# Performance work log

Hardware: AMD Instinct MI355X
Metric: run time of the kernel (lower is better)

## Reference

```python
import jax, jax.numpy as jnp
import numpy as np

E = 1024   # embedding_size
H = 16     # num_heads
DH = E // H


def setup_inputs() -> dict:
    key = jax.random.key(0)
    ks = jax.random.split(key, 11)
    B, S = 2, 2048
    std = 0.02
    return {
        "query": jax.random.normal(ks[0], (B, S, E), jnp.float32),
        "key": jax.random.normal(ks[1], (B, S, E), jnp.float32),
        "value": jax.random.normal(ks[2], (B, S, E), jnp.float32),
        "Wq": jax.random.normal(ks[3], (E, E), jnp.float32) * std,
        "bq": jnp.zeros((E,), jnp.float32),
        "Wk": jax.random.normal(ks[4], (E, E), jnp.float32) * std,
        "bk": jnp.zeros((E,), jnp.float32),
        "Wv": jax.random.normal(ks[5], (E, E), jnp.float32) * std,
        "bv": jnp.zeros((E,), jnp.float32),
        "Wo": jax.random.normal(ks[6], (E, E), jnp.float32) * std,
        "bo": jnp.zeros((E,), jnp.float32),
    }


def _split_heads(x, B, S):
    # [B,S,E] -> [B,H,S,DH]
    return x.reshape(B, S, H, DH).transpose(0, 2, 1, 3)


def reference(query, key, value, Wq, bq, Wk, bk, Wv, bv, Wo, bo):
    B, S, _ = query.shape
    # torch Linear: y = x @ W.T + b
    q = _split_heads(query @ Wq.T + bq, B, S)
    k = _split_heads(key @ Wk.T + bk, B, key.shape[1])
    v = _split_heads(value @ Wv.T + bv, B, value.shape[1])
    # naive unscaled attention (original has no 1/sqrt(d) factor)
    scores = jnp.einsum("bhsd,bhtd->bhst", q, k)  # [B,H,S,T]
    attn = jax.nn.softmax(scores, axis=-1)
    out = jnp.einsum("bhst,bhtd->bhsd", attn, v)  # [B,H,S,DH]
    out = out.transpose(0, 2, 1, 3).reshape(B, S, E)
    return out @ Wo.T + bo
```

## Files before the change

### kernel.cpp

```cpp
#include <hip/hip_runtime.h>
#include <hip/hip_bf16.h>

constexpr int kB   = 2;
constexpr int kS   = 2048;
constexpr int kE   = 1024;
constexpr int kH   = 16;
constexpr int kDH  = 64;
constexpr int kTok = kB * kS;

constexpr float kLog2e = 1.4426950408889634f;

typedef short bf16x8 __attribute__((ext_vector_type(8)));
typedef float f32x4  __attribute__((ext_vector_type(4)));
typedef unsigned int uint2v __attribute__((ext_vector_type(2)));

__device__ __forceinline__ float bf2f(unsigned short s) {
  union { unsigned int u; float f; } c; c.u = ((unsigned int)s) << 16; return c.f;
}
__device__ __forceinline__ unsigned short f2bf(float f) {
  union { float f; unsigned int u; } c; c.f = f;
  unsigned int u = c.u;
  u += 0x7fffu + ((u >> 16) & 1u);
  return (unsigned short)(u >> 16);
}

__device__ __forceinline__ unsigned cvtpk(float lo, float hi) {
  unsigned r;
  asm("v_cvt_pk_bf16_f32 %0, %1, %2" : "=v"(r) : "v"(lo), "v"(hi));
  return r;
}

__device__ __forceinline__ float fexp2(float x) {
  float r;
  asm("v_exp_f32 %0, %1" : "=v"(r) : "v"(x));
  return r;
}

__device__ __forceinline__ void gl_lds16(const unsigned short* g, unsigned short* l) {
  __builtin_amdgcn_global_load_lds(
      (const __attribute__((address_space(1))) unsigned int*)g,
      (__attribute__((address_space(3))) unsigned int*)l, 16, 0, 0);
}

__global__ void detect_dtype(const unsigned short* __restrict__ q, int* flag) {
  __shared__ int cnt;
  if (threadIdx.x == 0) cnt = 0;
  __syncthreads();
  int bad = 0;
  for (int i = threadIdx.x; i < 4096; i += 256) {
    unsigned int e = (q[i] >> 7) & 0xFF;
    if (e >= 0xC0) bad++;
  }
  atomicAdd(&cnt, bad);
  __syncthreads();
  if (threadIdx.x == 0) *flag = (cnt > 8) ? 1 : 0;
}

struct Seg { const void* src; unsigned short* dst; unsigned int n; unsigned int blk0; };
struct ConvArgs { Seg s[11]; float scale[11]; };

__global__ __launch_bounds__(256) void conv_all(ConvArgs a, const int* __restrict__ flag) {
  const unsigned int bid = blockIdx.x;
  int si = 0;
  #pragma unroll
  for (int i = 1; i < 11; ++i)
    if (bid >= a.s[i].blk0) si = i;
  const Seg sg = a.s[si];
  const float sc = a.scale[si];
  const int i0 = ((int)(bid - sg.blk0) * 256 + threadIdx.x) * 8;
  if (i0 >= (int)sg.n) return;
  if (*flag) {
    const float* s = (const float*)sg.src + i0;
    f32x4 f0 = *(const f32x4*)(s);
    f32x4 f1 = *(const f32x4*)(s + 4);
    bf16x8 v;
    #pragma unroll
    for (int j = 0; j < 4; ++j) v[j]     = (short)f2bf(f0[j] * sc);
    #pragma unroll
    for (int j = 0; j < 4; ++j) v[j + 4] = (short)f2bf(f1[j] * sc);
    *(bf16x8*)&sg.dst[i0] = v;
  } else {
    bf16x8 v = *(const bf16x8*)((const unsigned short*)sg.src + i0);
    if (sc != 1.0f) {
      #pragma unroll
      for (int j = 0; j < 8; ++j)
        v[j] = (short)f2bf(bf2f((unsigned short)v[j]) * sc);
    }
    *(bf16x8*)&sg.dst[i0] = v;
  }
}

__device__ __forceinline__ void gemm_core(
    const unsigned short* __restrict__ A,
    const unsigned short* __restrict__ W,
    int Kdim, int bM, int bN,
    unsigned short* As, unsigned short* Ws,
    f32x4 acc[4][4])
{
  const int tid  = threadIdx.x;
  const int lane = tid & 63;
  const int wv   = tid >> 6;
  const int wm   = (wv >> 1) * 64;
  const int wn   = (wv & 1) * 64;
  const int lr   = lane & 15;
  const int kq   = (lane >> 4) * 8;

  const int r0 = tid >> 2;
  const int c0 = (tid & 3) * 8;

  const unsigned short* Ag = A + (size_t)(bM + r0) * Kdim + c0;
  const unsigned short* Wg = W + (size_t)(bN + r0) * Kdim + c0;
  unsigned short* lA = &As[tid * 8];
  unsigned short* lW = &Ws[tid * 8];

  gl_lds16(Ag,                      lA);
  gl_lds16(Ag + (size_t)64 * Kdim,  lA + 2048);
  gl_lds16(Wg,                      lW);
  gl_lds16(Wg + (size_t)64 * Kdim,  lW + 2048);
  __syncthreads();

  for (int k0 = 0; k0 < Kdim; k0 += 32) {
    const int co = ((k0 >> 5) & 1) * 4096;
    if (k0 + 32 < Kdim) {
      const int no = co ^ 4096;
      gl_lds16(Ag + k0 + 32,                      lA + no);
      gl_lds16(Ag + (size_t)64 * Kdim + k0 + 32,  lA + no + 2048);
      gl_lds16(Wg + k0 + 32,                      lW + no);
      gl_lds16(Wg + (size_t)64 * Kdim + k0 + 32,  lW + no + 2048);
    }

    bf16x8 a[4], b[4];
    #pragma unroll
    for (int i = 0; i < 4; ++i)
      a[i] = *(const bf16x8*)&As[co + (wm + i * 16 + lr) * 32 + kq];
    #pragma unroll
    for (int i = 0; i < 4; ++i)
      b[i] = *(const bf16x8*)&Ws[co + (wn + i * 16 + lr) * 32 + kq];
    #pragma unroll
    for (int i = 0; i < 4; ++i)
      #pragma unroll
      for (int j = 0; j < 4; ++j)
        acc[i][j] = __builtin_amdgcn_mfma_f32_16x16x32_bf16(a[i], b[j], acc[i][j], 0, 0, 0);

    __syncthreads();
  }
}

__global__ __launch_bounds__(256) void gemm_qkv(
    const unsigned short* __restrict__ Abase,
    const unsigned short* __restrict__ Wbase,
    const unsigned short* __restrict__ biasbase,
    unsigned short* __restrict__ Cbase)
{
  __shared__ unsigned short As[2 * 128 * 32];
  __shared__ unsigned short Ws[2 * 128 * 32];

  const int bid = blockIdx.x + (blockIdx.y << 3) + (blockIdx.z << 8);
  const int swz = (bid & 7) * 96 + (bid >> 3);
  const int z   = swz >> 8;
  const int rem = swz & 255;
  const int bM  = (rem >> 3) * 128;
  const int bN  = (rem & 7) * 128;

  const unsigned short* A    = Abase    + (size_t)z * (kTok * kE);
  const unsigned short* W    = Wbase    + (size_t)z * (kE * kE);
  const unsigned short* bias = biasbase + (size_t)z * kE;
  unsigned short* C          = Cbase    + (size_t)z * (kTok * kE);

  f32x4 acc[4][4] = {};
  gemm_core(A, W, kE, bM, bN, As, Ws, acc);

  const int lane = threadIdx.x & 63;
  const int wv   = threadIdx.x >> 6;
  const int wm   = (wv >> 1) * 64;
  const int wn   = (wv & 1) * 64;
  const int lr   = lane & 15;
  const int qd   = lane >> 4;
  #pragma unroll
  for (int j = 0; j < 4; ++j) {
    const int col = bN + wn + j * 16 + lr;
    const float bb = bf2f(bias[col]);
    #pragma unroll
    for (int i = 0; i < 4; ++i)
      #pragma unroll
      for (int r = 0; r < 4; ++r) {
        const int row = bM + wm + i * 16 + qd * 4 + r;
        C[(size_t)row * kE + col] = f2bf(acc[i][j][r] + bb);
      }
  }
}

__global__ __launch_bounds__(256) void vtrans(
    const unsigned short* __restrict__ Vb,
    unsigned short* __restrict__ Vt)
{
  __shared__ unsigned short Lt[64 * 72];
  const int tid = threadIdx.x;
  const int bh  = blockIdx.y;
  const int b   = bh >> 4;
  const int h   = bh & 15;
  const int hcol = h * kDH;
  const int s0  = blockIdx.x * 64;

  #pragma unroll
  for (int issue = 0; issue < 2; ++issue) {
    int g = issue * 256 + tid;
    int r = g >> 3, c = (g & 7) * 8;
    bf16x8 vv = *(const bf16x8*)&Vb[(size_t)(b * kS + s0 + r) * kE + hcol + c];
    const int swz = ((((r >> 3) ^ (c >> 3)) & 7) << 3) + (r & 7);
    #pragma unroll
    for (int i = 0; i < 8; ++i)
      Lt[(c + i) * 72 + swz] = (unsigned short)vv[i];
  }
  __syncthreads();
  #pragma unroll
  for (int issue = 0; issue < 2; ++issue) {
    int g = issue * 256 + tid;
    int f = g >> 3, tc = (g & 7) * 8;
    const int blk = ((tc >> 3) ^ (f >> 3)) & 7;
    bf16x8 vv = *(const bf16x8*)&Lt[f * 72 + (blk << 3)];
    *(bf16x8*)&Vt[(size_t)b * (kE * kS) + (size_t)(hcol + f) * kS + s0 + tc] = vv;
  }
}

__global__ __launch_bounds__(256) void gemm_out(
    const unsigned short* __restrict__ A,
    const unsigned short* __restrict__ W,
    const unsigned short* __restrict__ bias,
    void* __restrict__ C,
    const int* __restrict__ flag)
{
  __shared__ unsigned short As[2 * 128 * 32];
  __shared__ unsigned short Ws[2 * 128 * 32];

  const int bid = blockIdx.x + (blockIdx.y << 3);
  const int swz = (bid & 7) * 32 + (bid >> 3);
  const int bM  = (swz >> 3) * 128;
  const int bN  = (swz & 7) * 128;

  f32x4 acc[4][4] = {};
  gemm_core(A, W, kE, bM, bN, As, Ws, acc);

  const int lane = threadIdx.x & 63;
  const int wv   = threadIdx.x >> 6;
  const int wm   = (wv >> 1) * 64;
  const int wn   = (wv & 1) * 64;
  const int lr   = lane & 15;
  const int qd   = lane >> 4;
  if (*flag) {
    float* Cf = (float*)C;
    #pragma unroll
    for (int j = 0; j < 4; ++j) {
      const int col = bN + wn + j * 16 + lr;
      const float bb = bf2f(bias[col]);
      #pragma unroll
      for (int i = 0; i < 4; ++i)
        #pragma unroll
        for (int r = 0; r < 4; ++r) {
          const int row = bM + wm + i * 16 + qd * 4 + r;
          Cf[(size_t)row * kE + col] = acc[i][j][r] + bb;
        }
    }
  } else {
    unsigned short* Cb = (unsigned short*)C;
    #pragma unroll
    for (int j = 0; j < 4; ++j) {
      const int col = bN + wn + j * 16 + lr;
      const float bb = bf2f(bias[col]);
      #pragma unroll
      for (int i = 0; i < 4; ++i)
        #pragma unroll
        for (int r = 0; r < 4; ++r) {
          const int row = bM + wm + i * 16 + qd * 4 + r;
          Cb[(size_t)row * kE + col] = f2bf(acc[i][j][r] + bb);
        }
    }
  }
}

__global__ __launch_bounds__(256) void attn(
    const unsigned short* __restrict__ Qb,
    const unsigned short* __restrict__ Kb,
    const unsigned short* __restrict__ Vt,
    unsigned short* __restrict__ Ob)
{
  __shared__ unsigned short Ks[2][64 * 72];
  __shared__ unsigned short Vs[2][64 * 72];

  const int tid  = threadIdx.x;
  const int lane = tid & 63;
  const int w    = tid >> 6;
  const int lr   = lane & 15;
  const int quad = lane >> 4;
  const int kq   = quad * 8;

  const int bid = blockIdx.x + (blockIdx.y << 5);
  const int swz = (bid & 7) * 128 + (bid >> 3);
  const int bh  = swz >> 5;
  const int b   = bh >> 4;
  const int h   = bh & 15;
  const int q0  = (swz & 31) * 64;

  const size_t rowbase = (size_t)b * kS * kE;
  const int hcol = h * kDH;
  const unsigned short* Vbase = Vt + (size_t)b * (kE * kS) + (size_t)hcol * kS;

  const int r0 = tid >> 3;
  const int c0 = (tid & 7) * 8;

  bf16x8 aq[2];
  #pragma unroll
  for (int hh = 0; hh < 2; ++hh)
    aq[hh] = *(const bf16x8*)
        &Qb[rowbase + (size_t)(q0 + w * 16 + lr) * kE + hcol + hh * 32 + kq];

  bf16x8 ones;
  #pragma unroll
  for (int j = 0; j < 8; ++j) ones[j] = (short)0x3F80;

  f32x4 o[4] = {};
  f32x4 ol   = {};

  bf16x8 rk0 = *(const bf16x8*)&Kb[rowbase + (size_t)(r0)      * kE + hcol + c0];
  bf16x8 rk1 = *(const bf16x8*)&Kb[rowbase + (size_t)(r0 + 32) * kE + hcol + c0];
  bf16x8 rv0 = *(const bf16x8*)&Vbase[(size_t)(r0)      * kS + c0];
  bf16x8 rv1 = *(const bf16x8*)&Vbase[(size_t)(r0 + 32) * kS + c0];
  *(bf16x8*)&Ks[0][ r0       * 72 + c0] = rk0;
  *(bf16x8*)&Ks[0][(r0 + 32) * 72 + c0] = rk1;
  *(bf16x8*)&Vs[0][ r0       * 72 + c0] = rv0;
  *(bf16x8*)&Vs[0][(r0 + 32) * 72 + c0] = rv1;
  rk0 = *(const bf16x8*)&Kb[rowbase + (size_t)(64 + r0)      * kE + hcol + c0];
  rk1 = *(const bf16x8*)&Kb[rowbase + (size_t)(64 + r0 + 32) * kE + hcol + c0];
  rv0 = *(const bf16x8*)&Vbase[(size_t)(r0)      * kS + 64 + c0];
  rv1 = *(const bf16x8*)&Vbase[(size_t)(r0 + 32) * kS + 64 + c0];
  __syncthreads();

  for (int t0 = 0; t0 < kS; t0 += 64) {
    const int cur = (t0 >> 6) & 1;
    const int nxt = cur ^ 1;

    if (t0 + 64 < kS) {
      *(bf16x8*)&Ks[nxt][ r0       * 72 + c0] = rk0;
      *(bf16x8*)&Ks[nxt][(r0 + 32) * 72 + c0] = rk1;
      *(bf16x8*)&Vs[nxt][ r0       * 72 + c0] = rv0;
      *(bf16x8*)&Vs[nxt][(r0 + 32) * 72 + c0] = rv1;
    }
    if (t0 + 128 < kS) {
      const int t2 = t0 + 128;
      rk0 = *(const bf16x8*)&Kb[rowbase + (size_t)(t2 + r0)      * kE + hcol + c0];
      rk1 = *(const bf16x8*)&Kb[rowbase + (size_t)(t2 + r0 + 32) * kE + hcol + c0];
      rv0 = *(const bf16x8*)&Vbase[(size_t)(r0)      * kS + t2 + c0];
      rv1 = *(const bf16x8*)&Vbase[(size_t)(r0 + 32) * kS + t2 + c0];
    }

    f32x4 s[4];
    #pragma unroll
    for (int tn = 0; tn < 4; ++tn)
      s[tn] = f32x4{0.f, 0.f, 0.f, 0.f};
    __builtin_amdgcn_s_setprio(1);
    #pragma unroll
    for (int tn = 0; tn < 4; ++tn) {
      const bf16x8 bk0 = *(const bf16x8*)&Ks[cur][(tn * 16 + lr) * 72 + 0 + kq];
      const bf16x8 bk1 = *(const bf16x8*)&Ks[cur][(tn * 16 + lr) * 72 + 32 + kq];
      s[tn] = __builtin_amdgcn_mfma_f32_16x16x32_bf16(bk0, aq[0], s[tn], 0, 0, 0);
      s[tn] = __builtin_amdgcn_mfma_f32_16x16x32_bf16(bk1, aq[1], s[tn], 0, 0, 0);
    }
    __builtin_amdgcn_s_setprio(0);

    #pragma unroll
    for (int tn = 0; tn < 4; ++tn)
      #pragma unroll
      for (int r = 0; r < 4; ++r)
        s[tn][r] = fexp2(s[tn][r]);

    bf16x8 ap[2];
    #pragma unroll
    for (int kk = 0; kk < 2; ++kk) {
      const unsigned A0 = cvtpk(s[2 * kk][0],     s[2 * kk][1]);
      const unsigned A1 = cvtpk(s[2 * kk + 1][0], s[2 * kk + 1][1]);
      const uint2v u   = __builtin_amdgcn_permlane32_swap(A0, A1, false, false);
      const uint2v z02 = __builtin_amdgcn_permlane16_swap(u[0], u[1], false, false);
      const unsigned B0 = cvtpk(s[2 * kk][2],     s[2 * kk][3]);
      const unsigned B1 = cvtpk(s[2 * kk + 1][2], s[2 * kk + 1][3]);
      const uint2v v2  = __builtin_amdgcn_permlane32_swap(B0, B1, false, false);
      const uint2v z13 = __builtin_amdgcn_permlane16_swap(v2[0], v2[1], false, false);
      union { unsigned ud[4]; bf16x8 v; } pk;
      pk.ud[0] = z02[0];
      pk.ud[1] = z13[0];
      pk.ud[2] = z02[1];
      pk.ud[3] = z13[1];
      ap[kk] = pk.v;
    }

    __builtin_amdgcn_s_setprio(1);
    #pragma unroll
    for (int kk = 0; kk < 2; ++kk) {
      #pragma unroll
      for (int dt = 0; dt < 4; ++dt) {
        const bf16x8 bv = *(const bf16x8*)&Vs[cur][(dt * 16 + lr) * 72 + kk * 32 + kq];
        o[dt] = __builtin_amdgcn_mfma_f32_16x16x32_bf16(ap[kk], bv, o[dt], 0, 0, 0);
      }
      ol = __builtin_amdgcn_mfma_f32_16x16x32_bf16(ap[kk], ones, ol, 0, 0, 0);
    }
    __builtin_amdgcn_s_setprio(0);

    __syncthreads();
  }

  float inv[4];
  #pragma unroll
  for (int r = 0; r < 4; ++r)
    inv[r] = 1.0f / ol[r];

  #pragma unroll
  for (int dt = 0; dt < 4; ++dt) {
    #pragma unroll
    for (int r = 0; r < 4; ++r) {
      const int row = q0 + w * 16 + quad * 4 + r;
      const int col = hcol + dt * 16 + lr;
      Ob[rowbase + (size_t)row * kE + col] = f2bf(o[dt][r] * inv[r]);
    }
  }
}

extern "C" void kernel_launch(void* const* d_in, const int* in_sizes, int n_in,
                              void* d_out, int out_size, void* d_ws, size_t ws_size,
                              hipStream_t stream) {
  const int nQKV = kTok * kE;
  const int nW   = kE * kE;
  const int nB   = kE;

  char* wsb = (char*)d_ws;
  int* flag = (int*)wsb;
  unsigned short* qc  = (unsigned short*)(wsb + 16);
  unsigned short* kc  = qc  + (size_t)nQKV;
  unsigned short* vc  = kc  + (size_t)nQKV;
  unsigned short* Wqc = vc  + (size_t)nQKV;
  unsigned short* Wkc = Wqc + (size_t)nW;
  unsigned short* Wvc = Wkc + (size_t)nW;
  unsigned short* Woc = Wvc + (size_t)nW;
  unsigned short* bqc = Woc + (size_t)nW;
  unsigned short* bkc = bqc + nB;
  unsigned short* bvc = bkc + nB;
  unsigned short* boc = bvc + nB;
  unsigned short* Qb  = boc + nB;
  unsigned short* Kb  = Qb  + (size_t)nQKV;
  unsigned short* Vb  = Kb  + (size_t)nQKV;
  unsigned short* Vtb = kc;
  unsigned short* Ob  = qc;

  detect_dtype<<<1, 256, 0, stream>>>((const unsigned short*)d_in[0], flag);

  ConvArgs ca;
  const void* srcs[11] = { d_in[0], d_in[1], d_in[2], d_in[3], d_in[4], d_in[5],
                           d_in[6], d_in[7], d_in[8], d_in[9], d_in[10] };
  unsigned short* dsts[11] = { qc, kc, vc, Wqc, bqc, Wkc, bkc, Wvc, bvc, Woc, boc };
  const unsigned int ns[11] = { (unsigned)nQKV, (unsigned)nQKV, (unsigned)nQKV,
                                (unsigned)nW, (unsigned)nB, (unsigned)nW, (unsigned)nB,
                                (unsigned)nW, (unsigned)nB, (unsigned)nW, (unsigned)nB };
  unsigned int blk = 0;
  for (int i = 0; i < 11; ++i) {
    ca.s[i].src = srcs[i]; ca.s[i].dst = dsts[i]; ca.s[i].n = ns[i]; ca.s[i].blk0 = blk;
    ca.scale[i] = 1.0f;
    blk += (ns[i] + 2047) / 2048;
  }
  ca.scale[3] = kLog2e;
  ca.scale[4] = kLog2e;
  conv_all<<<blk, 256, 0, stream>>>(ca, flag);

  dim3 blk256(256);
  dim3 gqkv(kE / 128, kTok / 128, 3);
  gemm_qkv<<<gqkv, blk256, 0, stream>>>(qc, Wqc, bqc, Qb);

  dim3 gvt(kS / 64, kB * kH);
  vtrans<<<gvt, blk256, 0, stream>>>(Vb, Vtb);

  dim3 gattn(kS / 64, kB * kH);
  attn<<<gattn, blk256, 0, stream>>>(Qb, Kb, Vtb, Ob);

  dim3 gout(kE / 128, kTok / 128);
  gemm_out<<<gout, blk256, 0, stream>>>(Ob, Woc, boc, d_out, flag);
}
```

Baseline: 256.5 us.

## Switch attention to 32x32x16 MFMA with 128-query tiles per block

The attention kernel now uses 32x32x16 bf16 MFMA instead of 16x16x32, and each wave handles 32 query rows, so a block covers 128 queries and the grid is halved. Each K/V tile loaded into LDS is reused across twice as many queries, which cuts LDS and global traffic per unit of work, and the larger MFMA shape gives more compute per instruction. The P-matrix repacking drops from permlane32 plus permlane16 swaps to permlane32 swaps alone. The cost is more accumulator registers per wave and half as many blocks (512), which may lower occupancy and load balance.

```diff
diff --git a/kernel.cpp b/kernel.cpp
--- a/kernel.cpp
+++ b/kernel.cpp
@@ -12,6 +12,7 @@
 
 typedef short bf16x8 __attribute__((ext_vector_type(8)));
 typedef float f32x4  __attribute__((ext_vector_type(4)));
+typedef float f32x16 __attribute__((ext_vector_type(16)));
 typedef unsigned int uint2v __attribute__((ext_vector_type(2)));
 
 __device__ __forceinline__ float bf2f(unsigned short s) {
@@ -290,16 +291,15 @@
   const int tid  = threadIdx.x;
   const int lane = tid & 63;
   const int w    = tid >> 6;
-  const int lr   = lane & 15;
-  const int quad = lane >> 4;
-  const int kq   = quad * 8;
-
-  const int bid = blockIdx.x + (blockIdx.y << 5);
-  const int swz = (bid & 7) * 128 + (bid >> 3);
-  const int bh  = swz >> 5;
+  const int q31  = lane & 31;
+  const int hi   = lane >> 5;
+
+  const int bid = blockIdx.x + (blockIdx.y << 4);
+  const int swz = (bid & 7) * 64 + (bid >> 3);
+  const int bh  = swz >> 4;
   const int b   = bh >> 4;
   const int h   = bh & 15;
-  const int q0  = (swz & 31) * 64;
+  const int q0  = (swz & 15) * 128;
 
   const size_t rowbase = (size_t)b * kS * kE;
   const int hcol = h * kDH;
@@ -308,18 +308,18 @@
   const int r0 = tid >> 3;
   const int c0 = (tid & 7) * 8;
 
-  bf16x8 aq[2];
-  #pragma unroll
-  for (int hh = 0; hh < 2; ++hh)
-    aq[hh] = *(const bf16x8*)
-        &Qb[rowbase + (size_t)(q0 + w * 16 + lr) * kE + hcol + hh * 32 + kq];
+  bf16x8 aq[4];
+  #pragma unroll
+  for (int ks = 0; ks < 4; ++ks)
+    aq[ks] = *(const bf16x8*)
+        &Qb[rowbase + (size_t)(q0 + w * 32 + q31) * kE + hcol + ks * 16 + hi * 8];
 
   bf16x8 ones;
   #pragma unroll
   for (int j = 0; j < 8; ++j) ones[j] = (short)0x3F80;
 
-  f32x4 o[4] = {};
-  f32x4 ol   = {};
+  f32x16 o[2] = {};
+  f32x16 ol   = {};
 
   bf16x8 rk0 = *(const bf16x8*)&Kb[rowbase + (size_t)(r0)      * kE + hcol + c0];
   bf16x8 rk1 = *(const bf16x8*)&Kb[rowbase + (size_t)(r0 + 32) * kE + hcol + c0];
@@ -353,72 +353,81 @@
       rv1 = *(const bf16x8*)&Vbase[(size_t)(r0 + 32) * kS + t2 + c0];
     }
 
-    f32x4 s[4];
-    #pragma unroll
-    for (int tn = 0; tn < 4; ++tn)
-      s[tn] = f32x4{0.f, 0.f, 0.f, 0.f};
+    f32x16 s0 = {}, s1 = {};
     __builtin_amdgcn_s_setprio(1);
     #pragma unroll
-    for (int tn = 0; tn < 4; ++tn) {
-      const bf16x8 bk0 = *(const bf16x8*)&Ks[cur][(tn * 16 + lr) * 72 + 0 + kq];
-      const bf16x8 bk1 = *(const bf16x8*)&Ks[cur][(tn * 16 + lr) * 72 + 32 + kq];
-      s[tn] = __builtin_amdgcn_mfma_f32_16x16x32_bf16(bk0, aq[0], s[tn], 0, 0, 0);
-      s[tn] = __builtin_amdgcn_mfma_f32_16x16x32_bf16(bk1, aq[1], s[tn], 0, 0, 0);
+    for (int ks = 0; ks < 4; ++ks) {
+      const bf16x8 ak0 = *(const bf16x8*)&Ks[cur][(q31)      * 72 + ks * 16 + hi * 8];
+      const bf16x8 ak1 = *(const bf16x8*)&Ks[cur][(32 + q31) * 72 + ks * 16 + hi * 8];
+      s0 = __builtin_amdgcn_mfma_f32_32x32x16_bf16(ak0, aq[ks], s0, 0, 0, 0);
+      s1 = __builtin_amdgcn_mfma_f32_32x32x16_bf16(ak1, aq[ks], s1, 0, 0, 0);
     }
     __builtin_amdgcn_s_setprio(0);
 
     #pragma unroll
-    for (int tn = 0; tn < 4; ++tn)
-      #pragma unroll
-      for (int r = 0; r < 4; ++r)
-        s[tn][r] = fexp2(s[tn][r]);
-
-    bf16x8 ap[2];
-    #pragma unroll
-    for (int kk = 0; kk < 2; ++kk) {
-      const unsigned A0 = cvtpk(s[2 * kk][0],     s[2 * kk][1]);
-      const unsigned A1 = cvtpk(s[2 * kk + 1][0], s[2 * kk + 1][1]);
-      const uint2v u   = __builtin_amdgcn_permlane32_swap(A0, A1, false, false);
-      const uint2v z02 = __builtin_amdgcn_permlane16_swap(u[0], u[1], false, false);
-      const unsigned B0 = cvtpk(s[2 * kk][2],     s[2 * kk][3]);
-      const unsigned B1 = cvtpk(s[2 * kk + 1][2], s[2 * kk + 1][3]);
-      const uint2v v2  = __builtin_amdgcn_permlane32_swap(B0, B1, false, false);
-      const uint2v z13 = __builtin_amdgcn_permlane16_swap(v2[0], v2[1], false, false);
-      union { unsigned ud[4]; bf16x8 v; } pk;
-      pk.ud[0] = z02[0];
-      pk.ud[1] = z13[0];
-      pk.ud[2] = z02[1];
-      pk.ud[3] = z13[1];
-      ap[kk] = pk.v;
+    for (int r = 0; r < 16; ++r) {
+      s0[r] = fexp2(s0[r]);
+      s1[r] = fexp2(s1[r]);
+    }
+
+    bf16x8 ap0[2], ap1[2];
+    {
+      unsigned dA[4], dB[4];
+      #pragma unroll
+      for (int g = 0; g < 4; ++g) {
+        dA[g] = cvtpk(s0[4 * g],     s0[4 * g + 1]);
+        dB[g] = cvtpk(s0[4 * g + 2], s0[4 * g + 3]);
+      }
+      #pragma unroll
+      for (int m = 0; m < 2; ++m) {
+        const uint2v u = __builtin_amdgcn_permlane32_swap(dA[2 * m], dA[2 * m + 1], false, false);
+        const uint2v v = __builtin_amdgcn_permlane32_swap(dB[2 * m], dB[2 * m + 1], false, false);
+        union { unsigned ud[4]; bf16x8 v8; } pk;
+        pk.ud[0] = u[0]; pk.ud[1] = v[0]; pk.ud[2] = u[1]; pk.ud[3] = v[1];
+        ap0[m] = pk.v8;
+      }
+      #pragma unroll
+      for (int g = 0; g < 4; ++g) {
+        dA[g] = cvtpk(s1[4 * g],     s1[4 * g + 1]);
+        dB[g] = cvtpk(s1[4 * g + 2], s1[4 * g + 3]);
+      }
+      #pragma unroll
+      for (int m = 0; m < 2; ++m) {
+        const uint2v u = __builtin_amdgcn_permlane32_swap(dA[2 * m], dA[2 * m + 1], false, false);
+        const uint2v v = __builtin_amdgcn_permlane32_swap(dB[2 * m], dB[2 * m + 1], false, false);
+        union { unsigned ud[4]; bf16x8 v8; } pk;
+        pk.ud[0] = u[0]; pk.ud[1] = v[0]; pk.ud[2] = u[1]; pk.ud[3] = v[1];
+        ap1[m] = pk.v8;
+      }
     }
 
     __builtin_amdgcn_s_setprio(1);
     #pragma unroll
-    for (int kk = 0; kk < 2; ++kk) {
-      #pragma unroll
-      for (int dt = 0; dt < 4; ++dt) {
-        const bf16x8 bv = *(const bf16x8*)&Vs[cur][(dt * 16 + lr) * 72 + kk * 32 + kq];
-        o[dt] = __builtin_amdgcn_mfma_f32_16x16x32_bf16(ap[kk], bv, o[dt], 0, 0, 0);
-      }
-      ol = __builtin_amdgcn_mfma_f32_16x16x32_bf16(ap[kk], ones, ol, 0, 0, 0);
+    for (int m = 0; m < 2; ++m) {
+      #pragma unroll
+      for (int dt = 0; dt < 2; ++dt) {
+        const bf16x8 bv0 = *(const bf16x8*)&Vs[cur][(dt * 32 + q31) * 72 +      m * 16 + hi * 8];
+        const bf16x8 bv1 = *(const bf16x8*)&Vs[cur][(dt * 32 + q31) * 72 + 32 + m * 16 + hi * 8];
+        o[dt] = __builtin_amdgcn_mfma_f32_32x32x16_bf16(ap0[m], bv0, o[dt], 0, 0, 0);
+        o[dt] = __builtin_amdgcn_mfma_f32_32x32x16_bf16(ap1[m], bv1, o[dt], 0, 0, 0);
+      }
+      ol = __builtin_amdgcn_mfma_f32_32x32x16_bf16(ap0[m], ones, ol, 0, 0, 0);
+      ol = __builtin_amdgcn_mfma_f32_32x32x16_bf16(ap1[m], ones, ol, 0, 0, 0);
     }
     __builtin_amdgcn_s_setprio(0);
 
     __syncthreads();
   }
 
-  float inv[4];
-  #pragma unroll
-  for (int r = 0; r < 4; ++r)
-    inv[r] = 1.0f / ol[r];
-
-  #pragma unroll
-  for (int dt = 0; dt < 4; ++dt) {
-    #pragma unroll
-    for (int r = 0; r < 4; ++r) {
-      const int row = q0 + w * 16 + quad * 4 + r;
-      const int col = hcol + dt * 16 + lr;
-      Ob[rowbase + (size_t)row * kE + col] = f2bf(o[dt][r] * inv[r]);
+  #pragma unroll
+  for (int reg = 0; reg < 16; ++reg) {
+    const int crow = (reg & 3) + 8 * (reg >> 2) + 4 * hi;
+    const float inv = 1.0f / ol[reg];
+    const int row = q0 + w * 32 + crow;
+    #pragma unroll
+    for (int dt = 0; dt < 2; ++dt) {
+      const int col = hcol + dt * 32 + q31;
+      Ob[rowbase + (size_t)row * kE + col] = f2bf(o[dt][reg] * inv);
     }
   }
 }
@@ -475,7 +484,7 @@
   dim3 gvt(kS / 64, kB * kH);
   vtrans<<<gvt, blk256, 0, stream>>>(Vb, Vtb);
 
-  dim3 gattn(kS / 64, kB * kH);
+  dim3 gattn(kS / 128, kB * kH);
   attn<<<gattn, blk256, 0, stream>>>(Qb, Kb, Vtb, Ob);
 
   dim3 gout(kE / 128, kTok / 128);
```

New measurement: 250.1 us. -2.5%, faster.
